# Kernel optimization log

Hardware: AMD Instinct MI355X
Metric: run time of the kernel (lower is better)

The kernel has to match this reference:

```python
import jax, jax.numpy as jnp
from jax import lax
import numpy as np

B, H, W = 1024, 28, 28
EPS = 1e-5


def _conv(x, w, b):
    # 3x3, stride 1, pad 1, NCHW/OIHW
    y = lax.conv_general_dilated(x, w, (1, 1), ((1, 1), (1, 1)),
                                 dimension_numbers=('NCHW', 'OIHW', 'NCHW'))
    return y + b[None, :, None, None]


def _bn(x, g, b, m, v):
    # inference-mode batchnorm (affine with running stats)
    s = (g * lax.rsqrt(v + EPS))[None, :, None, None]
    return (x - m[None, :, None, None]) * s + b[None, :, None, None]


def _deform_sample(x, off):
    # x: [B,C,H,W], off: [B,18,H,W] ordered (y,x) per 3x3 tap
    Bs, C, Hs, Ws = x.shape
    off = off.reshape(Bs, 9, 2, Hs, Ws)
    k = jnp.arange(3, dtype=x.dtype) - 1.0
    ky = jnp.repeat(k, 3)  # [9]
    kx = jnp.tile(k, 3)    # [9]
    py = jnp.arange(Hs, dtype=x.dtype)[None, None, :, None] + ky[None, :, None, None] + off[:, :, 0]
    px = jnp.arange(Ws, dtype=x.dtype)[None, None, None, :] + kx[None, :, None, None] + off[:, :, 1]
    y0 = jnp.floor(py)
    x0 = jnp.floor(px)
    y1 = y0 + 1.0
    x1 = x0 + 1.0
    wy1 = py - y0
    wy0 = 1.0 - wy1
    wx1 = px - x0
    wx0 = 1.0 - wx1
    flat = x.reshape(Bs, C, Hs * Ws)

    def gather(yy, xx):
        valid = (yy >= 0) & (yy <= Hs - 1) & (xx >= 0) & (xx <= Ws - 1)
        yc = jnp.clip(yy, 0, Hs - 1).astype(jnp.int32)
        xc = jnp.clip(xx, 0, Ws - 1).astype(jnp.int32)
        idx = (yc * Ws + xc).reshape(Bs, -1)  # [B, 9*H*W]
        g = jax.vmap(lambda f, i: f[:, i])(flat, idx)  # [B, C, 9*H*W]
        return g.reshape(Bs, C, 9, Hs, Ws) * valid[:, None].astype(x.dtype)

    s = (gather(y0, x0) * (wy0 * wx0)[:, None]
         + gather(y0, x1) * (wy0 * wx1)[:, None]
         + gather(y1, x0) * (wy1 * wx0)[:, None]
         + gather(y1, x1) * (wy1 * wx1)[:, None])
    return s  # [B, C, 9, H, W]


def setup_inputs() -> dict:
    key = jax.random.key(0)
    ks = jax.random.split(key, 16)

    def rn(k, shape, s=0.05):
        return jax.random.normal(k, shape, jnp.float32) * s

    inp = {
        'x': jax.random.normal(ks[0], (B, 1, H, W), jnp.float32),
        'w_off': rn(ks[1], (18, 1, 3, 3)),
        'b_off': jnp.zeros((18,), jnp.float32),
        'w_dcn': rn(ks[2], (32, 1, 3, 3), 0.3),
        'b_dcn': rn(ks[3], (32,)),
        'w2': rn(ks[4], (64, 32, 3, 3), 0.06),
        'b2': rn(ks[5], (64,)),
        'w3': rn(ks[6], (128, 64, 3, 3), 0.04),
        'b3': rn(ks[7], (128,)),
        'w4': rn(ks[8], (128, 128, 3, 3), 0.03),
        'b4': rn(ks[9], (128,)),
        'w_fc': rn(ks[10], (10, 128), 0.09),
        'b_fc': rn(ks[11], (10,)),
    }
    chans = {'bn1': 32, 'bn2': 64, 'bn3': 128, 'bn4': 128}
    for i, (n, c) in enumerate(chans.items()):
        kk = jax.random.split(ks[12 + i], 4)
        inp[n + '_g'] = 1.0 + rn(kk[0], (c,), 0.1)
        inp[n + '_b'] = rn(kk[1], (c,), 0.1)
        inp[n + '_m'] = rn(kk[2], (c,), 0.1)
        inp[n + '_v'] = jax.random.uniform(kk[3], (c,), jnp.float32, 0.5, 1.5)
    return inp


def reference(x, w_off, b_off, w_dcn, b_dcn,
              bn1_g, bn1_b, bn1_m, bn1_v,
              w2, b2, bn2_g, bn2_b, bn2_m, bn2_v,
              w3, b3, bn3_g, bn3_b, bn3_m, bn3_v,
              w4, b4, bn4_g, bn4_b, bn4_m, bn4_v,
              w_fc, b_fc):
    off = _conv(x, w_off, b_off)                      # [B,18,H,W]
    s = _deform_sample(x, off)                        # [B,1,9,H,W]
    h = jnp.einsum('bckhw,ock->bohw', s, w_dcn.reshape(32, 1, 9))
    h = h + b_dcn[None, :, None, None]
    h = _bn(h, bn1_g, bn1_b, bn1_m, bn1_v)
    h = _bn(jax.nn.relu(_conv(h, w2, b2)), bn2_g, bn2_b, bn2_m, bn2_v)
    h = _bn(jax.nn.relu(_conv(h, w3, b3)), bn3_g, bn3_b, bn3_m, bn3_v)
    h = _bn(jax.nn.relu(_conv(h, w4, b4)), bn4_g, bn4_b, bn4_m, bn4_v)
    pooled = h.mean(axis=(2, 3))                      # avg_pool k=28 == global mean
    logits = pooled @ w_fc.T + b_fc
    return jax.nn.log_softmax(logits, axis=1)
```

## Files before the change

kernel.cpp:

```cpp
#include <hip/hip_runtime.h>
#include <hip/hip_bf16.h>

typedef __bf16 bf16x8 __attribute__((ext_vector_type(8)));
typedef float  f32x4  __attribute__((ext_vector_type(4)));

#define BN_EPS 1e-5f

constexpr size_t ACT_PER_IMG = 57600 + 115200 + 230400;
constexpr size_t SZ_POOL = (size_t)1024 * 128 * 4;
constexpr size_t SZ_W2   = (size_t)9 * 64 * 32 * 2;
constexpr size_t SZ_W3   = (size_t)9 * 128 * 64 * 2;
constexpr size_t SZ_W4   = (size_t)9 * 128 * 128 * 2;
constexpr size_t SZ_BN   = 704 * 4;
constexpr size_t SZ_FIXED = SZ_POOL + SZ_W2 + SZ_W3 + SZ_W4 + SZ_BN;

__device__ __forceinline__ unsigned pack2(float a, float b) {
    __hip_bfloat162 h = __float22bfloat162_rn(make_float2(a, b));
    union { __hip_bfloat162 h2; unsigned u; } u;
    u.h2 = h;
    return u.u;
}

struct PrepArgs {
    const float *w2, *w3, *w4;
    const float *g1, *b1, *m1, *v1;
    const float *g2, *b2, *m2, *v2;
    const float *g3, *b3, *m3, *v3;
    const float *g4, *b4, *m4, *v4;
    __hip_bfloat16 *W2, *W3, *W4;
    float *bn;
};

__global__ __launch_bounds__(256) void prep_k(PrepArgs a) {
    int idx = blockIdx.x * 256 + threadIdx.x;
    if (idx < 18432) {
        int e = idx & 7, lane = (idx >> 3) & 63, r = idx >> 9;
        int nb = r & 3, t = r >> 2;
        int o = nb * 16 + (lane & 15);
        int i = (lane >> 4) * 8 + e;
        a.W2[idx] = __float2bfloat16(a.w2[(o * 32 + i) * 9 + t]);
        return;
    }
    idx -= 18432;
    if (idx < 73728) {
        int e = idx & 7, lane = (idx >> 3) & 63, r = idx >> 9;
        int nb = r & 7, s = r >> 3;
        int kc = s & 1, t = s >> 1;
        int o = nb * 16 + (lane & 15);
        int i = kc * 32 + (lane >> 4) * 8 + e;
        a.W3[idx] = __float2bfloat16(a.w3[(o * 64 + i) * 9 + t]);
        return;
    }
    idx -= 73728;
    if (idx < 147456) {
        int e = idx & 7, lane = (idx >> 3) & 63, r = idx >> 9;
        int nb = r & 7, s = r >> 3;
        int kc = s & 3, t = s >> 2;
        int o = nb * 16 + (lane & 15);
        int i = kc * 32 + (lane >> 4) * 8 + e;
        a.W4[idx] = __float2bfloat16(a.w4[(o * 128 + i) * 9 + t]);
        return;
    }
    idx -= 147456;
    if (idx < 352) {
        const float *g, *bb, *mm, *vv; int c, so, cn;
        if (idx < 32)       { g = a.g1; bb = a.b1; mm = a.m1; vv = a.v1; c = idx;       so = 0;   cn = 32;  }
        else if (idx < 96)  { g = a.g2; bb = a.b2; mm = a.m2; vv = a.v2; c = idx - 32;  so = 64;  cn = 64;  }
        else if (idx < 224) { g = a.g3; bb = a.b3; mm = a.m3; vv = a.v3; c = idx - 96;  so = 192; cn = 128; }
        else                { g = a.g4; bb = a.b4; mm = a.m4; vv = a.v4; c = idx - 224; so = 448; cn = 128; }
        float s = g[c] * rsqrtf(vv[c] + BN_EPS);
        a.bn[so + c] = s;
        a.bn[so + cn + c] = bb[c] - mm[c] * s;
    }
}

__global__ __launch_bounds__(256) void deform_k(
    const float* __restrict__ x, const float* __restrict__ w_off,
    const float* __restrict__ b_off, const float* __restrict__ w_dcn,
    const float* __restrict__ b_dcn, const float* __restrict__ bn,
    __hip_bfloat16* __restrict__ act1, __hip_bfloat16* __restrict__ act2,
    __hip_bfloat16* __restrict__ act3, float* __restrict__ pooled, int b0)
{
    const int lb = blockIdx.x;
    const int b  = b0 + lb;
    const int tid = threadIdx.x;
    __shared__ float xp[900];
    __shared__ float sw[564];
    float* swo = sw;
    float* sbo = sw + 162;
    float* swd = sw + 180;
    float* sbd = sw + 468;
    float* ss1 = sw + 500;
    float* ssh = sw + 532;

    for (int i = tid; i < 900; i += 256) {
        int y = i / 30, xc = i % 30;
        float v = 0.f;
        if (y >= 1 && y <= 28 && xc >= 1 && xc <= 28)
            v = x[(size_t)b * 784 + (y - 1) * 28 + (xc - 1)];
        xp[i] = v;
    }
    for (int i = tid; i < 564; i += 256) {
        float v;
        if (i < 162)      v = w_off[i];
        else if (i < 180) v = b_off[i - 162];
        else if (i < 468) v = w_dcn[i - 180];
        else if (i < 500) v = b_dcn[i - 468];
        else if (i < 532) v = bn[i - 500];
        else              v = bn[32 + (i - 532)];
        sw[i] = v;
    }
    if (tid < 128) pooled[b * 128 + tid] = 0.f;
    __syncthreads();

    for (int p = tid; p < 784; p += 256) {
        int y = p / 28, xx = p % 28;
        float off[18];
        #pragma unroll
        for (int o = 0; o < 18; o++) off[o] = sbo[o];
        #pragma unroll
        for (int ty = 0; ty < 3; ty++)
            #pragma unroll
            for (int tx = 0; tx < 3; tx++) {
                float xv = xp[(y + ty) * 30 + (xx + tx)];
                int tap = ty * 3 + tx;
                #pragma unroll
                for (int o = 0; o < 18; o++) off[o] = fmaf(xv, swo[o * 9 + tap], off[o]);
            }
        float s[9];
        #pragma unroll
        for (int j = 0; j < 9; j++) {
            float py = (float)y + (float)(j / 3 - 1) + off[2 * j];
            float px = (float)xx + (float)(j % 3 - 1) + off[2 * j + 1];
            float y0 = floorf(py), x0 = floorf(px);
            float wy1 = py - y0, wx1 = px - x0;
            float wy0 = 1.f - wy1, wx0 = 1.f - wx1;
            float acc = 0.f;
            #pragma unroll
            for (int cy = 0; cy < 2; cy++)
                #pragma unroll
                for (int cx = 0; cx < 2; cx++) {
                    float yy = y0 + (float)cy, xf = x0 + (float)cx;
                    bool valid = (yy >= 0.f) && (yy <= 27.f) && (xf >= 0.f) && (xf <= 27.f);
                    int yc = (int)fminf(fmaxf(yy, 0.f), 27.f);
                    int xc = (int)fminf(fmaxf(xf, 0.f), 27.f);
                    float g = valid ? xp[(yc + 1) * 30 + (xc + 1)] : 0.f;
                    float w = (cy ? wy1 : wy0) * (cx ? wx1 : wx0);
                    acc = fmaf(g, w, acc);
                }
            s[j] = acc;
        }
        size_t base = ((size_t)lb * 900 + (size_t)(y + 1) * 30 + (xx + 1)) * 32;
        #pragma unroll
        for (int c0 = 0; c0 < 32; c0 += 8) {
            float h[8];
            #pragma unroll
            for (int ci = 0; ci < 8; ci++) {
                int c = c0 + ci;
                float hv = sbd[c];
                #pragma unroll
                for (int j = 0; j < 9; j++) hv = fmaf(s[j], swd[c * 9 + j], hv);
                h[ci] = hv * ss1[c] + ssh[c];
            }
            uint4 q;
            q.x = pack2(h[0], h[1]); q.y = pack2(h[2], h[3]);
            q.z = pack2(h[4], h[5]); q.w = pack2(h[6], h[7]);
            *reinterpret_cast<uint4*>(&act1[base + c0]) = q;
        }
    }

    for (int i = tid; i < 116; i += 256) {
        int py, px;
        if (i < 30)      { py = 0;          px = i; }
        else if (i < 60) { py = 29;         px = i - 30; }
        else if (i < 88) { py = i - 60 + 1; px = 0; }
        else             { py = i - 88 + 1; px = 29; }
        size_t pix = (size_t)lb * 900 + (size_t)py * 30 + px;
        uint4 z = {0, 0, 0, 0};
        uint4* p1 = reinterpret_cast<uint4*>(&act1[pix * 32]);
        #pragma unroll
        for (int k = 0; k < 4; k++) p1[k] = z;
        uint4* p2 = reinterpret_cast<uint4*>(&act2[pix * 64]);
        #pragma unroll
        for (int k = 0; k < 8; k++) p2[k] = z;
        uint4* p3 = reinterpret_cast<uint4*>(&act3[pix * 128]);
        #pragma unroll
        for (int k = 0; k < 16; k++) p3[k] = z;
    }
}

template<int CIN>
__device__ __forceinline__ int swz(int ofs) {
    if constexpr (CIN == 128) return (ofs >> 4) & 0x70;
    else if constexpr (CIN == 64) return (ofs >> 3) & 0x70;
    else return (ofs >> 2) & 0x30;
}

template<int COUT, int NFW>
__device__ __forceinline__ void loadWf(const __hip_bfloat16* __restrict__ Wt,
                                       int s, int nq, int lane, bf16x8 (&bf)[NFW]) {
    constexpr int NB = COUT / 16;
    #pragma unroll
    for (int nf = 0; nf < NFW; ++nf)
        bf[nf] = *reinterpret_cast<const bf16x8*>(
            Wt + (((size_t)s * NB + nq * NFW + nf) * 64 + lane) * 8);
}

template<int CIN>
__device__ __forceinline__ void loadAf(const __hip_bfloat16* tile,
                                       int s, const int (&pr)[7], const int (&pc)[7],
                                       int kg, bf16x8 (&af)[7]) {
    constexpr int KC = CIN / 32;
    int t = s / KC, kc = (s % KC) * 32;
    int ty = t / 3, tx = t % 3;
    #pragma unroll
    for (int mf = 0; mf < 7; ++mf) {
        int pix = (pr[mf] + ty) * 30 + (pc[mf] + tx);
        int ba = (pix * CIN + kc + kg * 8) * 2;
        ba ^= swz<CIN>(ba);
        af[mf] = *reinterpret_cast<const bf16x8*>(
            reinterpret_cast<const char*>(tile) + ba);
    }
}

template<int NFW>
__device__ __forceinline__ void mstep7(const bf16x8 (&af)[7], const bf16x8 (&wf)[NFW],
                                       f32x4 (&acc)[7][NFW]) {
    #pragma unroll
    for (int mf = 0; mf < 7; ++mf)
        #pragma unroll
        for (int nf = 0; nf < NFW; ++nf)
            acc[mf][nf] = __builtin_amdgcn_mfma_f32_16x16x32_bf16(
                af[mf], wf[nf], acc[mf][nf], 0, 0, 0);
}

template<int CIN, int COUT, bool POOL>
__device__ __forceinline__ void conv_body(
    const __hip_bfloat16* tile,
    const __hip_bfloat16* __restrict__ Wt,
    const float* __restrict__ bconv, const float* __restrict__ bnS,
    const float* __restrict__ bnB, __hip_bfloat16* __restrict__ aout,
    float* __restrict__ pooled, int lb, int gb, int rg, int lane, int nq)
{
    constexpr int KC  = CIN / 32;
    constexpr int NS  = 9 * KC;
    constexpr int NFW = COUT / 32;
    const int l15 = lane & 15, kg = lane >> 4;
    const int nbase = nq * (NFW * 16) + l15;

    int pr[7], pc[7];
    #pragma unroll
    for (int mf = 0; mf < 7; ++mf) {
        int m = mf * 16 + l15;
        pr[mf] = m / 28;
        pc[mf] = m % 28;
    }

    f32x4 acc[7][NFW] = {};
    bf16x8 wA[NFW], wB[NFW], aA[7], aB[7];

    loadWf<COUT, NFW>(Wt, 0, nq, lane, wA);
    loadAf<CIN>(tile, 0, pr, pc, kg, aA);
    loadWf<COUT, NFW>(Wt, 1, nq, lane, wB);
    loadAf<CIN>(tile, 1, pr, pc, kg, aB);

    #pragma unroll
    for (int s = 0; s < NS; s += 2) {
        __builtin_amdgcn_sched_barrier(0);
        mstep7<NFW>(aA, wA, acc);
        if (s + 2 < NS) {
            loadWf<COUT, NFW>(Wt, s + 2, nq, lane, wA);
            loadAf<CIN>(tile, s + 2, pr, pc, kg, aA);
        }
        __builtin_amdgcn_sched_barrier(0);
        if (s + 1 < NS) {
            mstep7<NFW>(aB, wB, acc);
            if (s + 3 < NS) {
                loadWf<COUT, NFW>(Wt, s + 3, nq, lane, wB);
                loadAf<CIN>(tile, s + 3, pr, pc, kg, aB);
            }
        }
    }

    if constexpr (!POOL) {
        #pragma unroll
        for (int mf = 0; mf < 7; ++mf) {
            #pragma unroll
            for (int nf = 0; nf < NFW; ++nf) {
                int n = nbase + nf * 16;
                float bc = bconv[n], sc = bnS[n], sh = bnB[n];
                #pragma unroll
                for (int r = 0; r < 4; r++) {
                    int m = mf * 16 + kg * 4 + r;
                    float y = acc[mf][nf][r] + bc;
                    y = fmaxf(y, 0.f);
                    y = y * sc + sh;
                    int oy = m / 28, ox = m % 28;
                    aout[((size_t)lb * 900 + (size_t)(rg * 4 + oy + 1) * 30 + (ox + 1)) * COUT + n]
                        = __float2bfloat16(y);
                }
            }
        }
    } else {
        #pragma unroll
        for (int nf = 0; nf < NFW; ++nf) {
            int n = nbase + nf * 16;
            float bc = bconv[n], sc = bnS[n], sh = bnB[n];
            float ps = 0.f;
            #pragma unroll
            for (int mf = 0; mf < 7; ++mf)
                #pragma unroll
                for (int r = 0; r < 4; r++) {
                    float y = acc[mf][nf][r] + bc;
                    y = fmaxf(y, 0.f);
                    ps += y * sc + sh;
                }
            ps += __shfl_xor(ps, 16, 64);
            ps += __shfl_xor(ps, 32, 64);
            if (lane < 16) atomicAdd(&pooled[gb * COUT + n], ps);
        }
    }
}

template<int CIN, int COUT, bool POOL>
__global__ __launch_bounds__(128, 2) void conv_k(
    const __hip_bfloat16* __restrict__ ain,
    const __hip_bfloat16* __restrict__ Wt,
    const float* __restrict__ bconv,
    const float* __restrict__ bnS,
    const float* __restrict__ bnB,
    __hip_bfloat16* __restrict__ aout,
    float* __restrict__ pooled, int b0, int nimg)
{
    __shared__ __align__(16) __hip_bfloat16 tile[180 * CIN];
    const int tid = threadIdx.x;
    const int lane = tid & 63;
    const int nq = tid >> 6;

    int rg, lb;
    {
        int flat = blockIdx.x + 7 * blockIdx.y;
        if ((nimg & 7) == 0) {
            int xcd = flat & 7, idx = flat >> 3;
            lb = xcd * (nimg >> 3) + idx / 7;
            rg = idx % 7;
        } else {
            rg = blockIdx.x; lb = blockIdx.y;
        }
    }

    const char* src = reinterpret_cast<const char*>(
        ain + ((size_t)lb * 900 + (size_t)rg * 120) * CIN);
    constexpr int TB = 180 * CIN * 2;
    for (int ofs = tid * 16; ofs < TB; ofs += 2048) {
        uint4 v = *reinterpret_cast<const uint4*>(src + ofs);
        *reinterpret_cast<uint4*>(reinterpret_cast<char*>(tile) + (ofs ^ swz<CIN>(ofs))) = v;
    }
    __syncthreads();

    conv_body<CIN, COUT, POOL>(tile, Wt, bconv, bnS, bnB, aout, pooled,
                               lb, b0 + lb, rg, lane, nq);
}

__global__ __launch_bounds__(256) void head_k(
    const float* __restrict__ pooled, const float* __restrict__ wfc,
    const float* __restrict__ bfc, float* __restrict__ out)
{
    int b = blockIdx.x * 4 + (threadIdx.x >> 6);
    int lane = threadIdx.x & 63;
    float m0 = pooled[b * 128 + lane] * (1.f / 784.f);
    float m1 = pooled[b * 128 + 64 + lane] * (1.f / 784.f);
    float lg[10];
    #pragma unroll
    for (int k = 0; k < 10; k++) {
        float p = m0 * wfc[k * 128 + lane] + m1 * wfc[k * 128 + 64 + lane];
        #pragma unroll
        for (int s2 = 32; s2 >= 1; s2 >>= 1) p += __shfl_xor(p, s2, 64);
        lg[k] = p + bfc[k];
    }
    float mx = lg[0];
    #pragma unroll
    for (int k = 1; k < 10; k++) mx = fmaxf(mx, lg[k]);
    float se = 0.f;
    #pragma unroll
    for (int k = 0; k < 10; k++) se += expf(lg[k] - mx);
    float lse = mx + logf(se);
    #pragma unroll
    for (int k = 0; k < 10; k++)
        if (lane == k) out[b * 10 + k] = lg[k] - lse;
}

extern "C" void kernel_launch(void* const* d_in, const int* in_sizes, int n_in,
                              void* d_out, int out_size, void* d_ws, size_t ws_size,
                              hipStream_t stream) {
    (void)in_sizes; (void)n_in; (void)out_size;
    const float* x     = (const float*)d_in[0];
    const float* w_off = (const float*)d_in[1];
    const float* b_off = (const float*)d_in[2];
    const float* w_dcn = (const float*)d_in[3];
    const float* b_dcn = (const float*)d_in[4];
    const float* w2    = (const float*)d_in[5];
    const float* b2    = (const float*)d_in[6];
    const float* w3    = (const float*)d_in[7];
    const float* b3    = (const float*)d_in[8];
    const float* w4    = (const float*)d_in[9];
    const float* b4    = (const float*)d_in[10];
    const float* w_fc  = (const float*)d_in[11];
    const float* b_fc  = (const float*)d_in[12];

    int CH = 256;
    while (CH > 1 && (size_t)CH * ACT_PER_IMG + SZ_FIXED > ws_size) CH >>= 1;
    const int NCHUNK = 1024 / CH;

    char* ws = (char*)d_ws;
    const size_t szA1 = (size_t)CH * 57600;
    const size_t szA2 = (size_t)CH * 115200;
    const size_t szA3 = (size_t)CH * 230400;
    __hip_bfloat16* act1 = (__hip_bfloat16*)(ws);
    __hip_bfloat16* act2 = (__hip_bfloat16*)(ws + szA1);
    __hip_bfloat16* act3 = (__hip_bfloat16*)(ws + szA1 + szA2);
    float* pooled        = (float*)(ws + szA1 + szA2 + szA3);
    __hip_bfloat16* W2   = (__hip_bfloat16*)(ws + szA1 + szA2 + szA3 + SZ_POOL);
    __hip_bfloat16* W3   = (__hip_bfloat16*)((char*)W2 + SZ_W2);
    __hip_bfloat16* W4   = (__hip_bfloat16*)((char*)W3 + SZ_W3);
    float* bn            = (float*)((char*)W4 + SZ_W4);

    PrepArgs pa;
    pa.w2 = w2; pa.w3 = w3; pa.w4 = w4;
    pa.g1 = (const float*)d_in[13]; pa.b1 = (const float*)d_in[14];
    pa.m1 = (const float*)d_in[15]; pa.v1 = (const float*)d_in[16];
    pa.g2 = (const float*)d_in[17]; pa.b2 = (const float*)d_in[18];
    pa.m2 = (const float*)d_in[19]; pa.v2 = (const float*)d_in[20];
    pa.g3 = (const float*)d_in[21]; pa.b3 = (const float*)d_in[22];
    pa.m3 = (const float*)d_in[23]; pa.v3 = (const float*)d_in[24];
    pa.g4 = (const float*)d_in[25]; pa.b4 = (const float*)d_in[26];
    pa.m4 = (const float*)d_in[27]; pa.v4 = (const float*)d_in[28];
    pa.W2 = W2; pa.W3 = W3; pa.W4 = W4; pa.bn = bn;

    prep_k<<<938, 256, 0, stream>>>(pa);
    for (int c = 0; c < NCHUNK; ++c) {
        int b0 = c * CH;
        deform_k<<<CH, 256, 0, stream>>>(x, w_off, b_off, w_dcn, b_dcn, bn,
                                         act1, act2, act3, pooled, b0);
        conv_k<32, 64, false><<<dim3(7, CH), 128, 0, stream>>>(
            act1, W2, b2, bn + 64, bn + 128, act2, nullptr, b0, CH);
        conv_k<64, 128, false><<<dim3(7, CH), 128, 0, stream>>>(
            act2, W3, b3, bn + 192, bn + 320, act3, nullptr, b0, CH);
        conv_k<128, 128, true><<<dim3(7, CH), 128, 0, stream>>>(
            act3, W4, b4, bn + 448, bn + 576, nullptr, pooled, b0, CH);
    }
    head_k<<<256, 256, 0, stream>>>(pooled, w_fc, b_fc, (float*)d_out);
}
```

Baseline: 648.0 us.

## Split deform kernel per image across blocks and widen conv blocks to four waves

```diff
diff --git a/kernel.cpp b/kernel.cpp
--- a/kernel.cpp
+++ b/kernel.cpp
@@ -81,7 +81,8 @@
     __hip_bfloat16* __restrict__ act1, __hip_bfloat16* __restrict__ act2,
     __hip_bfloat16* __restrict__ act3, float* __restrict__ pooled, int b0)
 {
-    const int lb = blockIdx.x;
+    const int q  = blockIdx.x;
+    const int lb = blockIdx.y;
     const int b  = b0 + lb;
     const int tid = threadIdx.x;
     __shared__ float xp[900];
@@ -110,10 +111,11 @@
         else              v = bn[32 + (i - 532)];
         sw[i] = v;
     }
-    if (tid < 128) pooled[b * 128 + tid] = 0.f;
+    if (q == 0 && tid < 128) pooled[b * 128 + tid] = 0.f;
     __syncthreads();
 
-    for (int p = tid; p < 784; p += 256) {
+    if (tid < 196) {
+        int p = q * 196 + tid;
         int y = p / 28, xx = p % 28;
         float off[18];
         #pragma unroll
@@ -162,14 +164,15 @@
                 for (int j = 0; j < 9; j++) hv = fmaf(s[j], swd[c * 9 + j], hv);
                 h[ci] = hv * ss1[c] + ssh[c];
             }
-            uint4 q;
-            q.x = pack2(h[0], h[1]); q.y = pack2(h[2], h[3]);
-            q.z = pack2(h[4], h[5]); q.w = pack2(h[6], h[7]);
-            *reinterpret_cast<uint4*>(&act1[base + c0]) = q;
-        }
-    }
-
-    for (int i = tid; i < 116; i += 256) {
+            uint4 qv;
+            qv.x = pack2(h[0], h[1]); qv.y = pack2(h[2], h[3]);
+            qv.z = pack2(h[4], h[5]); qv.w = pack2(h[6], h[7]);
+            *reinterpret_cast<uint4*>(&act1[base + c0]) = qv;
+        }
+    }
+
+    if (tid < 29) {
+        int i = q * 29 + tid;
         int py, px;
         if (i < 30)      { py = 0;          px = i; }
         else if (i < 60) { py = 29;         px = i - 30; }
@@ -198,18 +201,18 @@
 
 template<int COUT, int NFW>
 __device__ __forceinline__ void loadWf(const __hip_bfloat16* __restrict__ Wt,
-                                       int s, int nq, int lane, bf16x8 (&bf)[NFW]) {
+                                       int s, int ng, int lane, bf16x8 (&bf)[NFW]) {
     constexpr int NB = COUT / 16;
     #pragma unroll
     for (int nf = 0; nf < NFW; ++nf)
         bf[nf] = *reinterpret_cast<const bf16x8*>(
-            Wt + (((size_t)s * NB + nq * NFW + nf) * 64 + lane) * 8);
+            Wt + (((size_t)s * NB + ng * NFW + nf) * 64 + lane) * 8);
 }
 
 template<int CIN>
-__device__ __forceinline__ void loadAf(const __hip_bfloat16* tile,
-                                       int s, const int (&pr)[7], const int (&pc)[7],
-                                       int kg, bf16x8 (&af)[7]) {
+__device__ __forceinline__ void loadAf7(const __hip_bfloat16* tile,
+                                        int s, const int (&pr)[7], const int (&pc)[7],
+                                        int kg, bf16x8 (&af)[7]) {
     constexpr int KC = CIN / 32;
     int t = s / KC, kc = (s % KC) * 32;
     int ty = t / 3, tx = t % 3;
@@ -234,7 +237,7 @@
                 af[mf], wf[nf], acc[mf][nf], 0, 0, 0);
 }
 
-template<int CIN, int COUT, bool POOL>
+template<int CIN, int COUT, int NWAVES, bool POOL>
 __device__ __forceinline__ void conv_body(
     const __hip_bfloat16* tile,
     const __hip_bfloat16* __restrict__ Wt,
@@ -244,7 +247,7 @@
 {
     constexpr int KC  = CIN / 32;
     constexpr int NS  = 9 * KC;
-    constexpr int NFW = COUT / 32;
+    constexpr int NFW = COUT / (16 * NWAVES);
     const int l15 = lane & 15, kg = lane >> 4;
     const int nbase = nq * (NFW * 16) + l15;
 
@@ -260,9 +263,9 @@
     bf16x8 wA[NFW], wB[NFW], aA[7], aB[7];
 
     loadWf<COUT, NFW>(Wt, 0, nq, lane, wA);
-    loadAf<CIN>(tile, 0, pr, pc, kg, aA);
+    loadAf7<CIN>(tile, 0, pr, pc, kg, aA);
     loadWf<COUT, NFW>(Wt, 1, nq, lane, wB);
-    loadAf<CIN>(tile, 1, pr, pc, kg, aB);
+    loadAf7<CIN>(tile, 1, pr, pc, kg, aB);
 
     #pragma unroll
     for (int s = 0; s < NS; s += 2) {
@@ -270,14 +273,14 @@
         mstep7<NFW>(aA, wA, acc);
         if (s + 2 < NS) {
             loadWf<COUT, NFW>(Wt, s + 2, nq, lane, wA);
-            loadAf<CIN>(tile, s + 2, pr, pc, kg, aA);
+            loadAf7<CIN>(tile, s + 2, pr, pc, kg, aA);
         }
         __builtin_amdgcn_sched_barrier(0);
         if (s + 1 < NS) {
             mstep7<NFW>(aB, wB, acc);
             if (s + 3 < NS) {
                 loadWf<COUT, NFW>(Wt, s + 3, nq, lane, wB);
-                loadAf<CIN>(tile, s + 3, pr, pc, kg, aB);
+                loadAf7<CIN>(tile, s + 3, pr, pc, kg, aB);
             }
         }
     }
@@ -322,8 +325,8 @@
     }
 }
 
-template<int CIN, int COUT, bool POOL>
-__global__ __launch_bounds__(128, 2) void conv_k(
+template<int CIN, int COUT, int NWAVES, bool POOL>
+__global__ __launch_bounds__(NWAVES * 64, 2) void conv_k(
     const __hip_bfloat16* __restrict__ ain,
     const __hip_bfloat16* __restrict__ Wt,
     const float* __restrict__ bconv,
@@ -352,14 +355,15 @@
     const char* src = reinterpret_cast<const char*>(
         ain + ((size_t)lb * 900 + (size_t)rg * 120) * CIN);
     constexpr int TB = 180 * CIN * 2;
-    for (int ofs = tid * 16; ofs < TB; ofs += 2048) {
+    constexpr int STEP = NWAVES * 64 * 16;
+    for (int ofs = tid * 16; ofs < TB; ofs += STEP) {
         uint4 v = *reinterpret_cast<const uint4*>(src + ofs);
         *reinterpret_cast<uint4*>(reinterpret_cast<char*>(tile) + (ofs ^ swz<CIN>(ofs))) = v;
     }
     __syncthreads();
 
-    conv_body<CIN, COUT, POOL>(tile, Wt, bconv, bnS, bnB, aout, pooled,
-                               lb, b0 + lb, rg, lane, nq);
+    conv_body<CIN, COUT, NWAVES, POOL>(tile, Wt, bconv, bnS, bnB, aout, pooled,
+                                       lb, b0 + lb, rg, lane, nq);
 }
 
 __global__ __launch_bounds__(256) void head_k(
@@ -440,13 +444,13 @@
     prep_k<<<938, 256, 0, stream>>>(pa);
     for (int c = 0; c < NCHUNK; ++c) {
         int b0 = c * CH;
-        deform_k<<<CH, 256, 0, stream>>>(x, w_off, b_off, w_dcn, b_dcn, bn,
-                                         act1, act2, act3, pooled, b0);
-        conv_k<32, 64, false><<<dim3(7, CH), 128, 0, stream>>>(
+        deform_k<<<dim3(4, CH), 256, 0, stream>>>(x, w_off, b_off, w_dcn, b_dcn, bn,
+                                                  act1, act2, act3, pooled, b0);
+        conv_k<32, 64, 2, false><<<dim3(7, CH), 128, 0, stream>>>(
             act1, W2, b2, bn + 64, bn + 128, act2, nullptr, b0, CH);
-        conv_k<64, 128, false><<<dim3(7, CH), 128, 0, stream>>>(
+        conv_k<64, 128, 4, false><<<dim3(7, CH), 256, 0, stream>>>(
             act2, W3, b3, bn + 192, bn + 320, act3, nullptr, b0, CH);
-        conv_k<128, 128, true><<<dim3(7, CH), 128, 0, stream>>>(
+        conv_k<128, 128, 4, true><<<dim3(7, CH), 256, 0, stream>>>(
             act3, W4, b4, bn + 448, bn + 576, nullptr, pooled, b0, CH);
     }
     head_k<<<256, 256, 0, stream>>>(pooled, w_fc, b_fc, (float*)d_out);
```

Measured after the change: 624.8 us. -3.6%, faster.
